# Kernel optimization log

Hardware: AMD Instinct MI355X
Metric: run time of the kernel (lower is better)

Reference implementation:

```python
import jax, jax.numpy as jnp
import numpy as np

KERNEL = 500
PAD_IDX = 256


def setup_inputs() -> dict:
    key = jax.random.key(0)
    ks = jax.random.split(key, 8)
    B, L = 8, 1_000_000
    x = jax.random.randint(ks[0], (B, L), 0, 257, dtype=jnp.int64)
    emb = jax.random.normal(ks[1], (257, 8), dtype=jnp.float32)
    emb = emb.at[PAD_IDX].set(0.0)  # padding_idx row is zero
    W1 = jax.random.normal(ks[2], (128, 8, KERNEL), dtype=jnp.float32) * 0.02
    b1 = jax.random.normal(ks[3], (128,), dtype=jnp.float32) * 0.02
    W2 = jax.random.normal(ks[4], (128, 8, KERNEL), dtype=jnp.float32) * 0.02
    b2 = jax.random.normal(ks[5], (128,), dtype=jnp.float32) * 0.02
    fcW = jax.random.normal(ks[6], (2, 128), dtype=jnp.float32) * 0.1
    fcb = jax.random.normal(ks[7], (2,), dtype=jnp.float32) * 0.1
    return {"x": x, "emb": emb, "W1": W1, "b1": b1, "W2": W2, "b2": b2, "fcW": fcW, "fcb": fcb}


def reference(x, emb, W1, b1, W2, b2, fcW, fcb):
    B, L = x.shape
    P = L // KERNEL  # non-overlapping patches (stride == kernel_size)
    # embedding with padding_idx semantics: output zero at pad positions
    e = emb[x] * (x != PAD_IDX)[..., None].astype(emb.dtype)  # [B, L, 8]
    patches = e.reshape(B, P, KERNEL, 8)                      # [B, P, K, C]
    # conv1d(k=stride=500) == patchified GEMM; weight layout [out, in, k]
    g1 = jnp.einsum('bpkc,ock->bpo', patches, W1) + b1        # [B, P, 128]
    g2 = jnp.einsum('bpkc,ock->bpo', patches, W2) + b2
    h = jax.nn.relu(g1 * jax.nn.sigmoid(g2))                  # GLU gate + relu
    m = jnp.max(h, axis=1)                                    # global max pool -> [B, 128]
    return m @ fcW.T + fcb                                    # [B, num_classes]
```

## Files before the change

kernel.cpp:

```cpp
#include <hip/hip_runtime.h>


typedef __attribute__((ext_vector_type(8))) short short8;
typedef __attribute__((ext_vector_type(4))) float f32x4;

__device__ __forceinline__ unsigned short f2b(float f) {
    union { float f; unsigned u; } un;
    un.f = f;
    unsigned u = un.u;
    return (unsigned short)((u + 0x7FFFu + ((u >> 16) & 1u)) >> 16);
}

__device__ __forceinline__ void gll4(const int* g, void* l) {
    __builtin_amdgcn_global_load_lds(
        (const __attribute__((address_space(1))) void*)g,
        (__attribute__((address_space(3))) void*)l, 4, 0, 0);
}

#define KT_COUNT 125
#define WS_BBLK_BYTES (KT_COUNT * 256 * 32 * 2)
#define WS_MWS_OFF WS_BBLK_BYTES

__global__ __launch_bounds__(256) void prep_weights(
        const float* __restrict__ W1, const float* __restrict__ W2,
        unsigned short* __restrict__ Bblk, float* __restrict__ m_ws) {
    int u  = blockIdx.x * 256 + threadIdx.x;
    int kt = u >> 8;
    int c  = u & 255;
    int grp = c >> 5, s = c & 31;
    const float* W = (s < 16) ? W1 : W2;
    int oo = grp * 16 + (s & 15);
    unsigned short v[4][8];
#pragma unroll
    for (int ch = 0; ch < 8; ++ch) {
        float4 w4 = *(const float4*)&W[oo * 4000 + ch * 500 + kt * 4];
        v[0][ch] = f2b(w4.x); v[1][ch] = f2b(w4.y);
        v[2][ch] = f2b(w4.z); v[3][ch] = f2b(w4.w);
    }
#pragma unroll
    for (int g = 0; g < 4; ++g) {
        uint4 pack;
        pack.x = (unsigned)v[g][0] | ((unsigned)v[g][1] << 16);
        pack.y = (unsigned)v[g][2] | ((unsigned)v[g][3] << 16);
        pack.z = (unsigned)v[g][4] | ((unsigned)v[g][5] << 16);
        pack.w = (unsigned)v[g][6] | ((unsigned)v[g][7] << 16);
        *(uint4*)&Bblk[u * 32 + g * 8] = pack;
    }
    if (blockIdx.x < 4) m_ws[blockIdx.x * 256 + threadIdx.x] = 0.f;
}

__global__ __launch_bounds__(64, 1) void malconv_main(
        const int* __restrict__ x, const float* __restrict__ emb,
        const float* __restrict__ b1, const float* __restrict__ b2,
        const unsigned short* __restrict__ Bblk, float* __restrict__ m_ws) {
    __shared__ __align__(16) unsigned short embb[257 * 8];
    __shared__ __align__(16) int xs[2][32][64];

    const int t = threadIdx.x;
    for (int e = t; e < 257 * 8; e += 64) embb[e] = f2b(emb[e]);

    const int w  = (blockIdx.x & 7) * 125 + (blockIdx.x >> 3);
    const int mt = w >> 2, nq = w & 3;
    const int m0 = mt * 64;

    const int quad = t >> 4, l16 = t & 15;

    const unsigned short* bbase = Bblk + (nq * 64 + l16) * 32 + quad * 8;

    const int* xrow = x + (m0 + t) * 500;

    auto stage = [&](int Sn) {
        int* dst0 = &xs[Sn & 1][0][0];
#pragma unroll
        for (int p = 0; p < 32; ++p) {
            int pe = Sn * 32 + p;
            if (pe > 499) pe = 499;
            gll4(xrow + pe, (void*)(dst0 + p * 64));
        }
    };

    f32x4 acc[4][4];
#pragma unroll
    for (int mi = 0; mi < 4; ++mi)
#pragma unroll
        for (int ni = 0; ni < 4; ++ni) {
            f32x4 z = {0.f, 0.f, 0.f, 0.f};
            acc[mi][ni] = z;
        }

    stage(0);
    __syncthreads();

    short8 bA[4], bB[4];
#pragma unroll
    for (int ni = 0; ni < 4; ++ni) {
        bA[ni] = *(const short8*)(bbase + 0 * 8192 + ni * 512);
        bB[ni] = *(const short8*)(bbase + 1 * 8192 + ni * 512);
    }

    auto step = [&](int kt, int kl, short8 (&B)[4], int cur) {
        int xv[4];
        short8 af[4];
#pragma unroll
        for (int mi = 0; mi < 4; ++mi)
            xv[mi] = xs[cur][kl * 4 + quad][mi * 16 + l16];
#pragma unroll
        for (int mi = 0; mi < 4; ++mi)
            af[mi] = *(const short8*)&embb[xv[mi] * 8];
#pragma unroll
        for (int mi = 0; mi < 4; ++mi)
#pragma unroll
            for (int ni = 0; ni < 4; ++ni)
                acc[mi][ni] = __builtin_amdgcn_mfma_f32_16x16x32_bf16(
                    af[mi], B[ni], acc[mi][ni], 0, 0, 0);
        const int ktn = (kt + 2 < KT_COUNT) ? kt + 2 : KT_COUNT - 1;
#pragma unroll
        for (int ni = 0; ni < 4; ++ni)
            B[ni] = *(const short8*)(bbase + ktn * 8192 + ni * 512);
    };

    for (int S = 0; S < 15; ++S) {
        stage(S + 1);
        const int cur = S & 1;
#pragma unroll
        for (int kp = 0; kp < 4; ++kp) {
            step(S * 8 + kp * 2,     kp * 2,     bA, cur);
            step(S * 8 + kp * 2 + 1, kp * 2 + 1, bB, cur);
        }
        __syncthreads();
    }
    step(120, 0, bA, 1);
    step(121, 1, bB, 1);
    step(122, 2, bA, 1);
    step(123, 3, bB, 1);
    step(124, 4, bA, 1);

    const int b0i = m0 / 2000;
    const int bsplit = (b0i + 1) * 2000;
    const bool crosses = (m0 + 63) >= bsplit;
#pragma unroll
    for (int p = 0; p < 2; ++p) {
        const int j = nq * 32 + p * 16 + l16;
        const float bb1 = b1[j], bb2 = b2[j];
        float mx0 = 0.f, mx1 = 0.f;
#pragma unroll
        for (int mi = 0; mi < 4; ++mi)
#pragma unroll
            for (int r = 0; r < 4; ++r) {
                int row = m0 + mi * 16 + quad * 4 + r;
                float g1 = acc[mi][2 * p][r] + bb1;
                float g2 = acc[mi][2 * p + 1][r] + bb2;
                float h = fmaxf(g1 / (1.f + __expf(-g2)), 0.f);
                if (row >= bsplit) mx1 = fmaxf(mx1, h);
                else               mx0 = fmaxf(mx0, h);
            }
        mx0 = fmaxf(mx0, __shfl_xor(mx0, 16));
        mx0 = fmaxf(mx0, __shfl_xor(mx0, 32));
        mx1 = fmaxf(mx1, __shfl_xor(mx1, 16));
        mx1 = fmaxf(mx1, __shfl_xor(mx1, 32));
        if (quad == 0) {
            atomicMax((int*)&m_ws[b0i * 128 + j], __float_as_int(mx0));
            if (crosses)
                atomicMax((int*)&m_ws[(b0i + 1) * 128 + j], __float_as_int(mx1));
        }
    }
}

__global__ void fc_kernel(const float* __restrict__ m_ws,
                          const float* __restrict__ fcW,
                          const float* __restrict__ fcb,
                          float* __restrict__ out) {
    int t = threadIdx.x;
    if (t < 16) {
        int b = t >> 1, j = t & 1;
        float s = 0.f;
        for (int o = 0; o < 128; ++o) s += m_ws[b * 128 + o] * fcW[j * 128 + o];
        out[t] = s + fcb[j];
    }
}

extern "C" void kernel_launch(void* const* d_in, const int* in_sizes, int n_in,
                              void* d_out, int out_size, void* d_ws, size_t ws_size,
                              hipStream_t stream) {
    const int*   x   = (const int*)d_in[0];
    const float* emb = (const float*)d_in[1];
    const float* W1  = (const float*)d_in[2];
    const float* b1  = (const float*)d_in[3];
    const float* W2  = (const float*)d_in[4];
    const float* b2  = (const float*)d_in[5];
    const float* fcW = (const float*)d_in[6];
    const float* fcb = (const float*)d_in[7];
    float* out = (float*)d_out;

    unsigned short* Bblk = (unsigned short*)d_ws;
    float* m_ws = (float*)((char*)d_ws + WS_MWS_OFF);

    prep_weights<<<125, 256, 0, stream>>>(W1, W2, Bblk, m_ws);
    malconv_main<<<1000, 64, 0, stream>>>(x, emb, b1, b2, Bblk, m_ws);
    fc_kernel<<<1, 64, 0, stream>>>(m_ws, fcW, fcb, out);
}
```

Before: 171.9 us.

## Stage bf16 weight tiles into LDS via async global_load_lds alongside token ids

The weight blocks are re-laid out so each k-step is contiguous across output columns. They are then streamed into a double-buffered LDS tile using 16-byte global_load_lds, in the same async stage as the token ids. This replaces the per-thread register prefetch of B fragments from global memory. The stage depth is halved to 16 k-positions with padded x rows, and the last 4 positions are handled by a direct-global tail step. The aim is to hide weight-load latency behind MFMA work, at the cost of more LDS traffic and roughly twice as many barriers.

```diff
diff --git a/kernel.cpp b/kernel.cpp
--- a/kernel.cpp
+++ b/kernel.cpp
@@ -16,9 +16,14 @@
         (const __attribute__((address_space(1))) void*)g,
         (__attribute__((address_space(3))) void*)l, 4, 0, 0);
 }
+__device__ __forceinline__ void gll16(const unsigned short* g, void* l) {
+    __builtin_amdgcn_global_load_lds(
+        (const __attribute__((address_space(1))) void*)g,
+        (__attribute__((address_space(3))) void*)l, 16, 0, 0);
+}
 
 #define KT_COUNT 125
-#define WS_BBLK_BYTES (KT_COUNT * 256 * 32 * 2)
+#define WS_BBLK_BYTES (KT_COUNT * 4 * 256 * 8 * 2)
 #define WS_MWS_OFF WS_BBLK_BYTES
 
 __global__ __launch_bounds__(256) void prep_weights(
@@ -44,7 +49,7 @@
         pack.y = (unsigned)v[g][2] | ((unsigned)v[g][3] << 16);
         pack.z = (unsigned)v[g][4] | ((unsigned)v[g][5] << 16);
         pack.w = (unsigned)v[g][6] | ((unsigned)v[g][7] << 16);
-        *(uint4*)&Bblk[u * 32 + g * 8] = pack;
+        *(uint4*)&Bblk[kt * 8192 + g * 2048 + c * 8] = pack;
     }
     if (blockIdx.x < 4) m_ws[blockIdx.x * 256 + threadIdx.x] = 0.f;
 }
@@ -54,7 +59,8 @@
         const float* __restrict__ b1, const float* __restrict__ b2,
         const unsigned short* __restrict__ Bblk, float* __restrict__ m_ws) {
     __shared__ __align__(16) unsigned short embb[257 * 8];
-    __shared__ __align__(16) int xs[2][32][64];
+    __shared__ __align__(16) int xs[2][16][66];
+    __shared__ __align__(16) unsigned short Bs[2][4][4][64][8];
 
     const int t = threadIdx.x;
     for (int e = t; e < 257 * 8; e += 64) embb[e] = f2b(emb[e]);
@@ -65,18 +71,20 @@
 
     const int quad = t >> 4, l16 = t & 15;
 
-    const unsigned short* bbase = Bblk + (nq * 64 + l16) * 32 + quad * 8;
-
-    const int* xrow = x + (m0 + t) * 500;
-
-    auto stage = [&](int Sn) {
-        int* dst0 = &xs[Sn & 1][0][0];
-#pragma unroll
-        for (int p = 0; p < 32; ++p) {
-            int pe = Sn * 32 + p;
-            if (pe > 499) pe = 499;
-            gll4(xrow + pe, (void*)(dst0 + p * 64));
-        }
+    const int* xsrc = x + (m0 + t) * 500;
+    const unsigned short* bsrc = Bblk + (nq * 64 + t) * 8;
+
+    auto stage = [&](int S) {
+        const int buf = S & 1;
+#pragma unroll
+        for (int p = 0; p < 16; ++p)
+            gll4(xsrc + S * 16 + p, (void*)&xs[buf][p][0]);
+#pragma unroll
+        for (int s = 0; s < 4; ++s)
+#pragma unroll
+            for (int j = 0; j < 4; ++j)
+                gll16(bsrc + (4 * S + s) * 8192 + j * 2048,
+                      (void*)&Bs[buf][s][j][0][0]);
     };
 
     f32x4 acc[4][4];
@@ -91,19 +99,15 @@
     stage(0);
     __syncthreads();
 
-    short8 bA[4], bB[4];
-#pragma unroll
-    for (int ni = 0; ni < 4; ++ni) {
-        bA[ni] = *(const short8*)(bbase + 0 * 8192 + ni * 512);
-        bB[ni] = *(const short8*)(bbase + 1 * 8192 + ni * 512);
-    }
-
-    auto step = [&](int kt, int kl, short8 (&B)[4], int cur) {
+    auto step = [&](int s, int buf) {
         int xv[4];
-        short8 af[4];
-#pragma unroll
-        for (int mi = 0; mi < 4; ++mi)
-            xv[mi] = xs[cur][kl * 4 + quad][mi * 16 + l16];
+        short8 af[4], bf[4];
+#pragma unroll
+        for (int mi = 0; mi < 4; ++mi)
+            xv[mi] = xs[buf][s * 4 + quad][mi * 16 + l16];
+#pragma unroll
+        for (int ni = 0; ni < 4; ++ni)
+            bf[ni] = *(const short8*)&Bs[buf][s][quad][ni * 16 + l16][0];
 #pragma unroll
         for (int mi = 0; mi < 4; ++mi)
             af[mi] = *(const short8*)&embb[xv[mi] * 8];
@@ -112,28 +116,35 @@
 #pragma unroll
             for (int ni = 0; ni < 4; ++ni)
                 acc[mi][ni] = __builtin_amdgcn_mfma_f32_16x16x32_bf16(
-                    af[mi], B[ni], acc[mi][ni], 0, 0, 0);
-        const int ktn = (kt + 2 < KT_COUNT) ? kt + 2 : KT_COUNT - 1;
+                    af[mi], bf[ni], acc[mi][ni], 0, 0, 0);
+    };
+
+    for (int S = 0; S < 31; ++S) {
+        if (S < 30) stage(S + 1);
+        const int buf = S & 1;
+        step(0, buf); step(1, buf); step(2, buf); step(3, buf);
+        __syncthreads();
+    }
+    {
+        int xv[4];
+        short8 af[4], bf[4];
+#pragma unroll
+        for (int mi = 0; mi < 4; ++mi)
+            xv[mi] = x[(m0 + mi * 16 + l16) * 500 + 496 + quad];
 #pragma unroll
         for (int ni = 0; ni < 4; ++ni)
-            B[ni] = *(const short8*)(bbase + ktn * 8192 + ni * 512);
-    };
-
-    for (int S = 0; S < 15; ++S) {
-        stage(S + 1);
-        const int cur = S & 1;
-#pragma unroll
-        for (int kp = 0; kp < 4; ++kp) {
-            step(S * 8 + kp * 2,     kp * 2,     bA, cur);
-            step(S * 8 + kp * 2 + 1, kp * 2 + 1, bB, cur);
-        }
-        __syncthreads();
-    }
-    step(120, 0, bA, 1);
-    step(121, 1, bB, 1);
-    step(122, 2, bA, 1);
-    step(123, 3, bB, 1);
-    step(124, 4, bA, 1);
+            bf[ni] = *(const short8*)(Bblk + 124 * 8192 + quad * 2048 +
+                                      (nq * 64 + ni * 16 + l16) * 8);
+#pragma unroll
+        for (int mi = 0; mi < 4; ++mi)
+            af[mi] = *(const short8*)&embb[xv[mi] * 8];
+#pragma unroll
+        for (int mi = 0; mi < 4; ++mi)
+#pragma unroll
+            for (int ni = 0; ni < 4; ++ni)
+                acc[mi][ni] = __builtin_amdgcn_mfma_f32_16x16x32_bf16(
+                    af[mi], bf[ni], acc[mi][ni], 0, 0, 0);
+    }
 
     const int b0i = m0 / 2000;
     const int bsplit = (b0i + 1) * 2000;
```

After: 224.9 us. +30.9%, slower.
